# Kernel optimization log

Measured on AMD Instinct MI355X. Metric: run time of the kernel, lower is better.

The kernel has to match this reference:

```python
import jax, jax.numpy as jnp
import numpy as np

HIDDEN = 1024
NUM_HEADS = 16
HEAD_DIM = HIDDEN // NUM_HEADS
B, S = 2, 2048


def setup_inputs() -> dict:
    key = jax.random.key(0)
    ks = jax.random.split(key, 7)
    scale = 1.0 / np.sqrt(HIDDEN)
    return {
        "hidden_states": jax.random.normal(ks[0], (B, S, HIDDEN), dtype=jnp.float32),
        "attention_mask": jnp.ones((B, S), dtype=jnp.float32),
        "Wq": jax.random.normal(ks[1], (HIDDEN, HIDDEN), dtype=jnp.float32) * scale,
        "bq": jax.random.normal(ks[2], (HIDDEN,), dtype=jnp.float32) * 0.02,
        "Wk": jax.random.normal(ks[3], (HIDDEN, HIDDEN), dtype=jnp.float32) * scale,
        "bk": jax.random.normal(ks[4], (HIDDEN,), dtype=jnp.float32) * 0.02,
        "Wv": jax.random.normal(ks[5], (HIDDEN, HIDDEN), dtype=jnp.float32) * scale,
        "bv": jax.random.normal(ks[6], (HIDDEN,), dtype=jnp.float32) * 0.02,
    }


def reference(hidden_states, attention_mask, Wq, bq, Wk, bk, Wv, bv):
    # Linear projections (W stored [in, out], equivalent to torch Linear).
    q = hidden_states @ Wq + bq  # [B,S,H]
    k = hidden_states @ Wk + bk
    v = hidden_states @ Wv + bv

    def split_heads(x):  # [B,S,H] -> [B,nh,S,hd]
        return x.reshape(B, S, NUM_HEADS, HEAD_DIM).transpose(0, 2, 1, 3)

    q, k, v = split_heads(q), split_heads(k), split_heads(v)

    scores = jnp.einsum("bhqd,bhkd->bhqk", q, k) / jnp.sqrt(
        jnp.asarray(HEAD_DIM, dtype=q.dtype))
    min_val = jnp.finfo(scores.dtype).min
    ext_mask = (1.0 - attention_mask[:, None, None, :]) * min_val  # [B,1,1,S]
    scores = scores + ext_mask
    probs = jax.nn.softmax(scores, axis=-1)  # eval mode: no dropout
    ctx = jnp.einsum("bhqk,bhkd->bhqd", probs, v)
    ctx = ctx.transpose(0, 2, 1, 3).reshape(B, S, HIDDEN)
    return ctx
```

## Files before the change

### kernel.cpp

```cpp
#include <hip/hip_runtime.h>
#include <hip/hip_bf16.h>
#include <cstddef>
#include <cstdint>

#define HID 1024
#define NHEADS 16
#define HDIM 64
#define BATCH 2
#define SEQ 2048
#define MROWS (BATCH * SEQ)
#define BHT (BATCH * NHEADS)

typedef __attribute__((ext_vector_type(8))) short s8v;
typedef __attribute__((ext_vector_type(4))) float f4v;

__device__ __forceinline__ unsigned short f2bf(float x) {
    union { float f; unsigned int u; } c; c.f = x;
    return (unsigned short)((c.u + 0x7fffu + ((c.u >> 16) & 1u)) >> 16);
}
__device__ __forceinline__ unsigned int pkbf(float a, float b) {
    __hip_bfloat162 h = __float22bfloat162_rn(float2{a, b});
    union { __hip_bfloat162 v; unsigned int u; } c; c.v = h; return c.u;
}
__device__ __forceinline__ float bflo(unsigned int w) {
    union { unsigned int u; float f; } c; c.u = w << 16; return c.f;
}
__device__ __forceinline__ float bfhi(unsigned int w) {
    union { unsigned int u; float f; } c; c.u = w & 0xffff0000u; return c.f;
}

__device__ __forceinline__ void lds_load16(void* lds, const void* g) {
    __builtin_amdgcn_global_load_lds(
        (const __attribute__((address_space(1))) void*)g,
        (__attribute__((address_space(3))) void*)lds, 16, 0, 0);
}

__global__ __launch_bounds__(256) void conv_fused_kernel(
    const float* __restrict__ hs,
    const float* __restrict__ Wq, const float* __restrict__ Wk,
    const float* __restrict__ Wv,
    unsigned short* __restrict__ Ah, unsigned short* __restrict__ WTh)
{
    if (blockIdx.x < 2048) {
        const int idx = (blockIdx.x * 256 + threadIdx.x) * 8;
        float4 v0 = *(const float4*)&hs[idx];
        float4 v1 = *(const float4*)&hs[idx + 4];
        union { unsigned int w[4]; } pk;
        pk.w[0] = pkbf(v0.x, v0.y);
        pk.w[1] = pkbf(v0.z, v0.w);
        pk.w[2] = pkbf(v1.x, v1.y);
        pk.w[3] = pkbf(v1.z, v1.w);
        *(uint4*)&Ah[idx] = *(uint4*)&pk;
    } else {
        const int bid = blockIdx.x - 2048;
        const int z = bid >> 8;
        const int rem = bid & 255;
        const float* W = (z == 0) ? Wq : (z == 1) ? Wk : Wv;
        unsigned short* th = WTh + (size_t)z * HID * HID;

        __shared__ float tile[64][65];
        const int t = threadIdx.x;
        const int kb = (rem >> 4) * 64, nb = (rem & 15) * 64;
        const int c4 = (t & 15) * 4;
        const int r0 = t >> 4;

#pragma unroll
        for (int i = 0; i < 4; ++i) {
            int r = r0 + i * 16;
            float4 v = *(const float4*)&W[(size_t)(kb + r) * HID + nb + c4];
            tile[r][c4 + 0] = v.x; tile[r][c4 + 1] = v.y;
            tile[r][c4 + 2] = v.z; tile[r][c4 + 3] = v.w;
        }
        __syncthreads();
#pragma unroll
        for (int i = 0; i < 4; ++i) {
            int n = r0 + i * 16;
            union { unsigned int w[2]; unsigned long long q; } pk;
            pk.w[0] = pkbf(tile[c4 + 0][n], tile[c4 + 1][n]);
            pk.w[1] = pkbf(tile[c4 + 2][n], tile[c4 + 3][n]);
            *(unsigned long long*)&th[(size_t)(nb + n) * HID + kb + c4] = pk.q;
        }
    }
}

#define QSCALE 0.18033688011112042f

__global__ __launch_bounds__(256, 2) void qkv_mfma_kernel(
    const unsigned short* __restrict__ Ah, const unsigned short* __restrict__ WTh,
    const float* __restrict__ bq, const float* __restrict__ bk,
    const float* __restrict__ bv,
    unsigned short* __restrict__ Qg, unsigned short* __restrict__ Khi,
    unsigned short* __restrict__ VTg)
{
    __shared__ unsigned short S[24576];
    unsigned short* AS = S;
    unsigned short* B0 = S + 8192;
    unsigned short* B1 = S + 16384;

    const int z2 = blockIdx.z;
    const int t = threadIdx.x;
    const int wave = t >> 6, lane = t & 63, quad = lane >> 4, l15 = lane & 15;
    const int sw = l15 & 7;
    const int wm = wave >> 1, wn = wave & 1;
    const int rowBase = blockIdx.x * 128;
    const int colBase = blockIdx.y * 128;

    const int srow8 = lane >> 3;
    const int sc    = lane & 7;

    const unsigned short* BhQ = WTh;
    const unsigned short* BhK = WTh + (size_t)HID * HID;
    const unsigned short* BhV = WTh + (size_t)2 * HID * HID;

    size_t goffA[4], goffB[4];
#pragma unroll
    for (int it = 0; it < 4; ++it) {
        const int row = (wave * 4 + it) * 8 + srow8;
        const int gx = (sc ^ (row & 7)) * 8;
        goffA[it] = (size_t)(rowBase + row) * HID + gx;
        goffB[it] = (size_t)(colBase + row) * HID + gx;
    }

    if (z2 == 0) {
        f4v accq[4][4], acck[4][4];
#pragma unroll
        for (int mf = 0; mf < 4; ++mf)
#pragma unroll
            for (int nf = 0; nf < 4; ++nf) {
                accq[mf][nf] = (f4v){0.f, 0.f, 0.f, 0.f};
                acck[mf][nf] = (f4v){0.f, 0.f, 0.f, 0.f};
            }

        for (int kt = 0; kt < HID / 64; ++kt) {
            const int k0 = kt * 64;
            __syncthreads();
#pragma unroll
            for (int it = 0; it < 4; ++it) {
                lds_load16(&AS[(wave * 4 + it) * 512], &Ah[goffA[it] + k0]);
                lds_load16(&B0[(wave * 4 + it) * 512], &BhQ[goffB[it] + k0]);
                lds_load16(&B1[(wave * 4 + it) * 512], &BhK[goffB[it] + k0]);
            }
            __syncthreads();

#pragma unroll
            for (int kk = 0; kk < 2; ++kk) {
                const int csw = ((kk * 4 + quad) ^ sw) * 8;
                s8v af[4], bfq[4], bfk[4];
#pragma unroll
                for (int mf = 0; mf < 4; ++mf)
                    af[mf] = *(const s8v*)&AS[(wm * 64 + mf * 16 + l15) * 64 + csw];
#pragma unroll
                for (int nf = 0; nf < 4; ++nf) {
                    bfq[nf] = *(const s8v*)&B0[(wn * 64 + nf * 16 + l15) * 64 + csw];
                    bfk[nf] = *(const s8v*)&B1[(wn * 64 + nf * 16 + l15) * 64 + csw];
                }
#pragma unroll
                for (int mf = 0; mf < 4; ++mf)
#pragma unroll
                    for (int nf = 0; nf < 4; ++nf) {
                        accq[mf][nf] = __builtin_amdgcn_mfma_f32_16x16x32_bf16(bfq[nf], af[mf], accq[mf][nf], 0, 0, 0);
                        acck[mf][nf] = __builtin_amdgcn_mfma_f32_16x16x32_bf16(bfk[nf], af[mf], acck[mf][nf], 0, 0, 0);
                    }
            }
        }

#pragma unroll
        for (int nf = 0; nf < 4; ++nf) {
            const int n0 = colBase + wn * 64 + nf * 16 + quad * 4;
            const float4 bbq = *(const float4*)&bq[n0];
            const float4 bbk = *(const float4*)&bk[n0];
            const int h = n0 >> 6, d0 = n0 & 63;
#pragma unroll
            for (int mf = 0; mf < 4; ++mf) {
                const int rw = rowBase + wm * 64 + mf * 16 + l15;
                const int b = rw >> 11;
                const int ss = rw & (SEQ - 1);
                const size_t base = ((size_t)(b * NHEADS + h) * SEQ + ss) * HDIM + d0;
                union { unsigned int w[2]; unsigned long long q; } pk;
                pk.w[0] = pkbf((accq[mf][nf][0] + bbq.x) * QSCALE, (accq[mf][nf][1] + bbq.y) * QSCALE);
                pk.w[1] = pkbf((accq[mf][nf][2] + bbq.z) * QSCALE, (accq[mf][nf][3] + bbq.w) * QSCALE);
                *(unsigned long long*)&Qg[base] = pk.q;
                pk.w[0] = pkbf(acck[mf][nf][0] + bbk.x, acck[mf][nf][1] + bbk.y);
                pk.w[1] = pkbf(acck[mf][nf][2] + bbk.z, acck[mf][nf][3] + bbk.w);
                *(unsigned long long*)&Khi[base] = pk.q;
            }
        }
    } else {
        f4v acc[4][4];
#pragma unroll
        for (int mf = 0; mf < 4; ++mf)
#pragma unroll
            for (int nf = 0; nf < 4; ++nf) acc[mf][nf] = (f4v){0.f, 0.f, 0.f, 0.f};

        for (int kt = 0; kt < HID / 64; ++kt) {
            const int k0 = kt * 64;
            __syncthreads();
#pragma unroll
            for (int it = 0; it < 4; ++it) {
                lds_load16(&AS[(wave * 4 + it) * 512], &Ah[goffA[it] + k0]);
                lds_load16(&B0[(wave * 4 + it) * 512], &BhV[goffB[it] + k0]);
            }
            __syncthreads();

#pragma unroll
            for (int kk = 0; kk < 2; ++kk) {
                const int csw = ((kk * 4 + quad) ^ sw) * 8;
                s8v af[4], bf[4];
#pragma unroll
                for (int mf = 0; mf < 4; ++mf)
                    af[mf] = *(const s8v*)&AS[(wm * 64 + mf * 16 + l15) * 64 + csw];
#pragma unroll
                for (int nf = 0; nf < 4; ++nf)
                    bf[nf] = *(const s8v*)&B0[(wn * 64 + nf * 16 + l15) * 64 + csw];
#pragma unroll
                for (int mf = 0; mf < 4; ++mf)
#pragma unroll
                    for (int nf = 0; nf < 4; ++nf)
                        acc[mf][nf] = __builtin_amdgcn_mfma_f32_16x16x32_bf16(af[mf], bf[nf], acc[mf][nf], 0, 0, 0);
            }
        }

#pragma unroll
        for (int nf = 0; nf < 4; ++nf) {
            const int n = colBase + wn * 64 + nf * 16 + l15;
            const float bb = bv[n];
            const int h = n >> 6, d = n & 63;
#pragma unroll
            for (int mf = 0; mf < 4; ++mf) {
                const int rw0 = rowBase + wm * 64 + mf * 16 + quad * 4;
                const int b = rw0 >> 11;
                const int s0 = rw0 & (SEQ - 1);
                union { unsigned int w[2]; unsigned long long q; } pk;
                pk.w[0] = pkbf(acc[mf][nf][0] + bb, acc[mf][nf][1] + bb);
                pk.w[1] = pkbf(acc[mf][nf][2] + bb, acc[mf][nf][3] + bb);
                *(unsigned long long*)&VTg[((size_t)(b * NHEADS + h) * HDIM + d) * SEQ + s0] = pk.q;
            }
        }
    }
}

#define BC 64

__global__ __launch_bounds__(256, 2) void attn_mfma_kernel(
    const unsigned short* __restrict__ Qg, const unsigned short* __restrict__ Khi,
    const unsigned short* __restrict__ VTg,
    const float* __restrict__ mask, float* __restrict__ out)
{
    __shared__ unsigned short Kb[2][BC * HDIM];
    __shared__ unsigned short Vb[2][BC * HDIM];
    __shared__ unsigned short Pbuf[4][32 * BC];

    const int t = threadIdx.x;
    const int wave = t >> 6, lane = t & 63, quad = lane >> 4, l15 = lane & 15;
    const int sw = l15 & 7;
    const int bh = blockIdx.x, b = bh >> 4, h = bh & (NHEADS - 1);
    const int qbase = blockIdx.y * 128 + wave * 32;

    const size_t hb = (size_t)bh * SEQ * HDIM;
    const unsigned short* kbase = Khi + hb;
    const unsigned short* vbase = VTg + hb;
    const float* mrow = mask + b * SEQ;

    s8v qh[2][2];
#pragma unroll
    for (int qf = 0; qf < 2; ++qf)
#pragma unroll
        for (int ds = 0; ds < 2; ++ds) {
            size_t off = hb + (size_t)(qbase + qf * 16 + l15) * HDIM + ds * 32 + quad * 8;
            qh[qf][ds] = *(const s8v*)&Qg[off];
        }

    f4v oacc[2][4];
#pragma unroll
    for (int qf = 0; qf < 2; ++qf)
#pragma unroll
        for (int nf = 0; nf < 4; ++nf) oacc[qf][nf] = (f4v){0.f, 0.f, 0.f, 0.f};
    float l_r[2] = {0.f, 0.f};

    const int srow8 = lane >> 3;
    const int sc    = lane & 7;
    int koff[2], voff[2];
#pragma unroll
    for (int it = 0; it < 2; ++it) {
        const int row = (wave * 2 + it) * 8 + srow8;
        const int gx = (sc ^ (row & 7)) * 8;
        koff[it] = row * HDIM + gx;
        voff[it] = row * SEQ + gx;
    }

#pragma unroll
    for (int it = 0; it < 2; ++it) {
        const int i = wave * 2 + it;
        lds_load16(&Kb[0][i * 512], kbase + koff[it]);
        lds_load16(&Vb[0][i * 512], vbase + voff[it]);
    }
    __syncthreads();

    for (int kt = 0; kt < SEQ / BC; ++kt) {
        const int cur = kt & 1;
        if (kt + 1 < SEQ / BC) {
            const int nxt = cur ^ 1;
#pragma unroll
            for (int it = 0; it < 2; ++it) {
                const int i = wave * 2 + it;
                lds_load16(&Kb[nxt][i * 512], kbase + (kt + 1) * BC * HDIM + koff[it]);
                lds_load16(&Vb[nxt][i * 512], vbase + (kt + 1) * BC + voff[it]);
            }
        }
        float4 msv[4];
#pragma unroll
        for (int mf = 0; mf < 4; ++mf)
            msv[mf] = *(const float4*)&mrow[kt * BC + mf * 16 + quad * 4];

        f4v sacc[2][4];
#pragma unroll
        for (int qf = 0; qf < 2; ++qf)
#pragma unroll
            for (int mf = 0; mf < 4; ++mf) sacc[qf][mf] = (f4v){0.f, 0.f, 0.f, 0.f};
#pragma unroll
        for (int mf = 0; mf < 4; ++mf) {
#pragma unroll
            for (int ds = 0; ds < 2; ++ds) {
                s8v kh = *(const s8v*)&Kb[cur][(mf * 16 + l15) * HDIM + (((ds * 4 + quad) ^ sw) * 8)];
#pragma unroll
                for (int qf = 0; qf < 2; ++qf)
                    sacc[qf][mf] = __builtin_amdgcn_mfma_f32_16x16x32_bf16(kh, qh[qf][ds], sacc[qf][mf], 0, 0, 0);
            }
        }

#pragma unroll
        for (int qf = 0; qf < 2; ++qf) {
            float psum = 0.f;
            const int prow = (qf * 16 + l15) * BC;
#pragma unroll
            for (int mf = 0; mf < 4; ++mf) {
                const float* mp = (const float*)&msv[mf];
                float p0 = __builtin_amdgcn_exp2f(sacc[qf][mf][0]) * mp[0];
                float p1 = __builtin_amdgcn_exp2f(sacc[qf][mf][1]) * mp[1];
                float p2 = __builtin_amdgcn_exp2f(sacc[qf][mf][2]) * mp[2];
                float p3 = __builtin_amdgcn_exp2f(sacc[qf][mf][3]) * mp[3];
                union { unsigned int w[2]; unsigned long long q; } pk;
                pk.w[0] = pkbf(p0, p1);
                pk.w[1] = pkbf(p2, p3);
                psum += bflo(pk.w[0]) + bfhi(pk.w[0]) + bflo(pk.w[1]) + bfhi(pk.w[1]);
                const int c16 = (mf * 2 + (quad >> 1)) ^ sw;
                *(unsigned long long*)&Pbuf[wave][prow + c16 * 8 + (quad & 1) * 4] = pk.q;
            }
            l_r[qf] += psum;
        }

#pragma unroll
        for (int ks = 0; ks < 2; ++ks) {
            const int csw = ((ks * 4 + quad) ^ sw) * 8;
            s8v pa0 = *(const s8v*)&Pbuf[wave][(0 * 16 + l15) * BC + csw];
            s8v pa1 = *(const s8v*)&Pbuf[wave][(1 * 16 + l15) * BC + csw];
#pragma unroll
            for (int nf = 0; nf < 4; ++nf) {
                s8v vb = *(const s8v*)&Vb[cur][(nf * 16 + l15) * BC + csw];
                oacc[0][nf] = __builtin_amdgcn_mfma_f32_16x16x32_bf16(pa0, vb, oacc[0][nf], 0, 0, 0);
                oacc[1][nf] = __builtin_amdgcn_mfma_f32_16x16x32_bf16(pa1, vb, oacc[1][nf], 0, 0, 0);
            }
        }
        __syncthreads();
    }

#pragma unroll
    for (int qf = 0; qf < 2; ++qf) {
        float v = l_r[qf];
        v += __shfl_xor(v, 16);
        v += __shfl_xor(v, 32);
        float lv[4];
#pragma unroll
        for (int r = 0; r < 4; ++r)
            lv[r] = 1.0f / __shfl(v, quad * 4 + r);
#pragma unroll
        for (int nf = 0; nf < 4; ++nf)
#pragma unroll
            for (int r = 0; r < 4; ++r) {
                int q = qbase + qf * 16 + quad * 4 + r;
                int d = nf * 16 + l15;
                out[((size_t)b * SEQ + q) * HID + h * HDIM + d] = oacc[qf][nf][r] * lv[r];
            }
    }
}

extern "C" void kernel_launch(void* const* d_in, const int* in_sizes, int n_in,
                              void* d_out, int out_size, void* d_ws, size_t ws_size,
                              hipStream_t stream) {
    const float* hs   = (const float*)d_in[0];
    const float* mask = (const float*)d_in[1];
    const float* Wq   = (const float*)d_in[2];
    const float* bq   = (const float*)d_in[3];
    const float* Wk   = (const float*)d_in[4];
    const float* bk   = (const float*)d_in[5];
    const float* Wv   = (const float*)d_in[6];
    const float* bv   = (const float*)d_in[7];
    float* out = (float*)d_out;

    const size_t N = (size_t)MROWS * HID;
    unsigned short* Qg  = (unsigned short*)d_ws;
    unsigned short* Khi = Qg + N;
    unsigned short* VTg = Qg + 2 * N;
    unsigned short* Ah  = Qg + 3 * N;
    unsigned short* WTh = Qg + 4 * N;

    conv_fused_kernel<<<2048 + 768, 256, 0, stream>>>(hs, Wq, Wk, Wv, Ah, WTh);

    dim3 g1(MROWS / 128, HID / 128, 2);
    qkv_mfma_kernel<<<g1, 256, 0, stream>>>(Ah, WTh, bq, bk, bv, Qg, Khi, VTg);

    dim3 g2(BHT, SEQ / 128);
    attn_mfma_kernel<<<g2, 256, 0, stream>>>(Qg, Khi, VTg, mask, out);
}
```

Before: 175.1 us.

## Keep attention probabilities in registers via permlane swaps and fold mask into scores

The attention kernel no longer writes P to a per-wave LDS buffer and reads it back. It builds the bf16 A-operand fragments directly in registers using permlane32/permlane16 swaps. The mask is precomputed as an additive log-domain bias in the conversion kernel and used as the initial MFMA accumulator, which replaces the multiply after exp. s_setprio hints are also placed around the MFMA blocks. The row sum now uses the unrounded fp32 exponentials instead of bf16-rounded values, so normalization differs slightly, and the register-fragment layout must match the MFMA operand mapping exactly.

After: 169.6 us. 3.1% less time.

```diff
diff --git a/kernel.cpp b/kernel.cpp
--- a/kernel.cpp
+++ b/kernel.cpp
@@ -13,20 +13,11 @@
 
 typedef __attribute__((ext_vector_type(8))) short s8v;
 typedef __attribute__((ext_vector_type(4))) float f4v;
-
-__device__ __forceinline__ unsigned short f2bf(float x) {
-    union { float f; unsigned int u; } c; c.f = x;
-    return (unsigned short)((c.u + 0x7fffu + ((c.u >> 16) & 1u)) >> 16);
-}
+typedef __attribute__((ext_vector_type(2))) unsigned int u2v;
+
 __device__ __forceinline__ unsigned int pkbf(float a, float b) {
     __hip_bfloat162 h = __float22bfloat162_rn(float2{a, b});
     union { __hip_bfloat162 v; unsigned int u; } c; c.v = h; return c.u;
-}
-__device__ __forceinline__ float bflo(unsigned int w) {
-    union { unsigned int u; float f; } c; c.u = w << 16; return c.f;
-}
-__device__ __forceinline__ float bfhi(unsigned int w) {
-    union { unsigned int u; float f; } c; c.u = w & 0xffff0000u; return c.f;
 }
 
 __device__ __forceinline__ void lds_load16(void* lds, const void* g) {
@@ -36,10 +27,11 @@
 }
 
 __global__ __launch_bounds__(256) void conv_fused_kernel(
-    const float* __restrict__ hs,
+    const float* __restrict__ hs, const float* __restrict__ mask,
     const float* __restrict__ Wq, const float* __restrict__ Wk,
     const float* __restrict__ Wv,
-    unsigned short* __restrict__ Ah, unsigned short* __restrict__ WTh)
+    unsigned short* __restrict__ Ah, unsigned short* __restrict__ WTh,
+    float* __restrict__ lmask)
 {
     if (blockIdx.x < 2048) {
         const int idx = (blockIdx.x * 256 + threadIdx.x) * 8;
@@ -51,7 +43,7 @@
         pk.w[2] = pkbf(v1.x, v1.y);
         pk.w[3] = pkbf(v1.z, v1.w);
         *(uint4*)&Ah[idx] = *(uint4*)&pk;
-    } else {
+    } else if (blockIdx.x < 2816) {
         const int bid = blockIdx.x - 2048;
         const int z = bid >> 8;
         const int rem = bid & 255;
@@ -80,6 +72,9 @@
             pk.w[1] = pkbf(tile[c4 + 2][n], tile[c4 + 3][n]);
             *(unsigned long long*)&th[(size_t)(nb + n) * HID + kb + c4] = pk.q;
         }
+    } else {
+        const int idx = (blockIdx.x - 2816) * 256 + threadIdx.x;
+        lmask[idx] = (mask[idx] - 1.0f) * 1e30f;
     }
 }
 
@@ -244,11 +239,10 @@
 __global__ __launch_bounds__(256, 2) void attn_mfma_kernel(
     const unsigned short* __restrict__ Qg, const unsigned short* __restrict__ Khi,
     const unsigned short* __restrict__ VTg,
-    const float* __restrict__ mask, float* __restrict__ out)
+    const float* __restrict__ lmask, float* __restrict__ out)
 {
     __shared__ unsigned short Kb[2][BC * HDIM];
     __shared__ unsigned short Vb[2][BC * HDIM];
-    __shared__ unsigned short Pbuf[4][32 * BC];
 
     const int t = threadIdx.x;
     const int wave = t >> 6, lane = t & 63, quad = lane >> 4, l15 = lane & 15;
@@ -259,7 +253,7 @@
     const size_t hb = (size_t)bh * SEQ * HDIM;
     const unsigned short* kbase = Khi + hb;
     const unsigned short* vbase = VTg + hb;
-    const float* mrow = mask + b * SEQ;
+    const float* mrow = lmask + b * SEQ;
 
     s8v qh[2][2];
 #pragma unroll
@@ -307,6 +301,7 @@
                 lds_load16(&Vb[nxt][i * 512], vbase + (kt + 1) * BC + voff[it]);
             }
         }
+
         float4 msv[4];
 #pragma unroll
         for (int mf = 0; mf < 4; ++mf)
@@ -316,7 +311,10 @@
 #pragma unroll
         for (int qf = 0; qf < 2; ++qf)
 #pragma unroll
-            for (int mf = 0; mf < 4; ++mf) sacc[qf][mf] = (f4v){0.f, 0.f, 0.f, 0.f};
+            for (int mf = 0; mf < 4; ++mf)
+                sacc[qf][mf] = (f4v){msv[mf].x, msv[mf].y, msv[mf].z, msv[mf].w};
+
+        __builtin_amdgcn_s_setprio(1);
 #pragma unroll
         for (int mf = 0; mf < 4; ++mf) {
 #pragma unroll
@@ -327,40 +325,51 @@
                     sacc[qf][mf] = __builtin_amdgcn_mfma_f32_16x16x32_bf16(kh, qh[qf][ds], sacc[qf][mf], 0, 0, 0);
             }
         }
-
+        __builtin_amdgcn_s_setprio(0);
+
+        s8v pa[2][2];
 #pragma unroll
         for (int qf = 0; qf < 2; ++qf) {
-            float psum = 0.f;
-            const int prow = (qf * 16 + l15) * BC;
+            unsigned int wlo[4], whi[4];
+            float ps = 0.f;
 #pragma unroll
             for (int mf = 0; mf < 4; ++mf) {
-                const float* mp = (const float*)&msv[mf];
-                float p0 = __builtin_amdgcn_exp2f(sacc[qf][mf][0]) * mp[0];
-                float p1 = __builtin_amdgcn_exp2f(sacc[qf][mf][1]) * mp[1];
-                float p2 = __builtin_amdgcn_exp2f(sacc[qf][mf][2]) * mp[2];
-                float p3 = __builtin_amdgcn_exp2f(sacc[qf][mf][3]) * mp[3];
-                union { unsigned int w[2]; unsigned long long q; } pk;
-                pk.w[0] = pkbf(p0, p1);
-                pk.w[1] = pkbf(p2, p3);
-                psum += bflo(pk.w[0]) + bfhi(pk.w[0]) + bflo(pk.w[1]) + bfhi(pk.w[1]);
-                const int c16 = (mf * 2 + (quad >> 1)) ^ sw;
-                *(unsigned long long*)&Pbuf[wave][prow + c16 * 8 + (quad & 1) * 4] = pk.q;
-            }
-            l_r[qf] += psum;
-        }
-
+                float e0 = __builtin_amdgcn_exp2f(sacc[qf][mf][0]);
+                float e1 = __builtin_amdgcn_exp2f(sacc[qf][mf][1]);
+                float e2 = __builtin_amdgcn_exp2f(sacc[qf][mf][2]);
+                float e3 = __builtin_amdgcn_exp2f(sacc[qf][mf][3]);
+                ps += (e0 + e1) + (e2 + e3);
+                wlo[mf] = pkbf(e0, e1);
+                whi[mf] = pkbf(e2, e3);
+            }
+            l_r[qf] += ps;
+#pragma unroll
+            for (int ks = 0; ks < 2; ++ks) {
+                unsigned int alo = wlo[ks * 2], blo = wlo[ks * 2 + 1];
+                unsigned int ahi = whi[ks * 2], bhi = whi[ks * 2 + 1];
+                u2v r;
+                r = __builtin_amdgcn_permlane32_swap(alo, blo, false, false); alo = r[0]; blo = r[1];
+                r = __builtin_amdgcn_permlane32_swap(ahi, bhi, false, false); ahi = r[0]; bhi = r[1];
+                r = __builtin_amdgcn_permlane16_swap(alo, blo, false, false); alo = r[0]; blo = r[1];
+                r = __builtin_amdgcn_permlane16_swap(ahi, bhi, false, false); ahi = r[0]; bhi = r[1];
+                union { unsigned int w[4]; s8v v; } up;
+                up.w[0] = alo; up.w[1] = ahi; up.w[2] = blo; up.w[3] = bhi;
+                pa[qf][ks] = up.v;
+            }
+        }
+
+        __builtin_amdgcn_s_setprio(1);
 #pragma unroll
         for (int ks = 0; ks < 2; ++ks) {
             const int csw = ((ks * 4 + quad) ^ sw) * 8;
-            s8v pa0 = *(const s8v*)&Pbuf[wave][(0 * 16 + l15) * BC + csw];
-            s8v pa1 = *(const s8v*)&Pbuf[wave][(1 * 16 + l15) * BC + csw];
 #pragma unroll
             for (int nf = 0; nf < 4; ++nf) {
                 s8v vb = *(const s8v*)&Vb[cur][(nf * 16 + l15) * BC + csw];
-                oacc[0][nf] = __builtin_amdgcn_mfma_f32_16x16x32_bf16(pa0, vb, oacc[0][nf], 0, 0, 0);
-                oacc[1][nf] = __builtin_amdgcn_mfma_f32_16x16x32_bf16(pa1, vb, oacc[1][nf], 0, 0, 0);
-            }
-        }
+                oacc[0][nf] = __builtin_amdgcn_mfma_f32_16x16x32_bf16(pa[0][ks], vb, oacc[0][nf], 0, 0, 0);
+                oacc[1][nf] = __builtin_amdgcn_mfma_f32_16x16x32_bf16(pa[1][ks], vb, oacc[1][nf], 0, 0, 0);
+            }
+        }
+        __builtin_amdgcn_s_setprio(0);
         __syncthreads();
     }
 
@@ -403,12 +412,13 @@
     unsigned short* VTg = Qg + 2 * N;
     unsigned short* Ah  = Qg + 3 * N;
     unsigned short* WTh = Qg + 4 * N;
-
-    conv_fused_kernel<<<2048 + 768, 256, 0, stream>>>(hs, Wq, Wk, Wv, Ah, WTh);
+    float* lmask = (float*)(WTh + (size_t)3 * HID * HID);
+
+    conv_fused_kernel<<<2048 + 768 + 16, 256, 0, stream>>>(hs, mask, Wq, Wk, Wv, Ah, WTh, lmask);
 
     dim3 g1(MROWS / 128, HID / 128, 2);
     qkv_mfma_kernel<<<g1, 256, 0, stream>>>(Ah, WTh, bq, bk, bv, Qg, Khi, VTg);
 
     dim3 g2(BHT, SEQ / 128);
-    attn_mfma_kernel<<<g2, 256, 0, stream>>>(Qg, Khi, VTg, mask, out);
-}
+    attn_mfma_kernel<<<g2, 256, 0, stream>>>(Qg, Khi, VTg, lmask, out);
+}
```
